# Performance work log

Measured on AMD Instinct MI355X. Metric: run time of the kernel, lower is better.

The kernel has to match this reference:

```python
import jax, jax.numpy as jnp
import numpy as np

S, B, C, H, W = 5, 2, 128, 24, 24
N_ITER = 3
BN_EPS = 1e-5


def conv2d(x, w, b, pad):
    # x: (N, Cin, H, W), w: (Cout, Cin, kh, kw)
    y = jax.lax.conv_general_dilated(
        x, w, (1, 1), [(pad, pad), (pad, pad)],
        dimension_numbers=('NCHW', 'OIHW', 'NCHW'))
    return y + b[None, :, None, None]


def setup_inputs() -> dict:
    key = jax.random.key(0)
    ks = jax.random.split(key, 8)
    sc = 0.03  # keep pre-softmax logits in a sane range
    d = {}
    d['x'] = jax.random.normal(ks[0], (S, B, C, H, W), jnp.float32) * 0.5
    d['Wf_w'] = jax.random.normal(ks[1], (C, C, 3, 3), jnp.float32) * sc
    d['Wf_b'] = jnp.zeros((C,), jnp.float32)
    d['Wh_w'] = jax.random.normal(ks[2], (C, C, 3, 3), jnp.float32) * sc
    d['Wh_b'] = jnp.zeros((C,), jnp.float32)
    d['Wl_w'] = jax.random.normal(ks[3], (C, C, 3, 3), jnp.float32) * sc
    d['Wl_b'] = jnp.zeros((C,), jnp.float32)
    d['alpha'] = jnp.ones((1,), jnp.float32)
    d['Wc'] = jax.random.normal(ks[4], (C, C), jnp.float32) * sc
    d['Wg_w'] = jax.random.normal(ks[5], (C, C, 3, 3), jnp.float32) * sc
    d['Wg_b'] = jnp.zeros((C,), jnp.float32)
    d['bn_gamma'] = jnp.ones((C,), jnp.float32)
    d['bn_beta'] = jnp.zeros((C,), jnp.float32)
    d['gru_zr_w'] = jax.random.normal(ks[6], (2 * C, 2 * C, 5, 5), jnp.float32) * sc
    d['gru_zr_b'] = jnp.zeros((2 * C,), jnp.float32)
    d['gru_h_w'] = jax.random.normal(ks[7], (C, 2 * C, 5, 5), jnp.float32) * sc
    d['gru_h_b'] = jnp.zeros((C,), jnp.float32)
    d['intra_w'] = jnp.full((1,), 0.5, jnp.float32)
    d['inter_w'] = jnp.full((1,), 0.5, jnp.float32)
    return d


def reference(x, Wf_w, Wf_b, Wh_w, Wh_b, Wl_w, Wl_b, alpha, Wc, Wg_w, Wg_b,
              bn_gamma, bn_beta, gru_zr_w, gru_zr_b, gru_h_w, gru_h_b,
              intra_w, inter_w):
    S_, B_, C_, H_, W_ = x.shape
    N = H_ * W_
    # BatchNorm2d in inference mode with fresh running stats (mean=0, var=1)
    bn_scale = bn_gamma / jnp.sqrt(1.0 + BN_EPS)
    mask = (1.0 - jnp.eye(S_, dtype=x.dtype))[:, :, None, None, None, None]
    h = x
    for _ in range(N_ITER):
        hb = h.reshape(S_ * B_, C_, H_, W_)
        # ---- intra-node self-attention (per node in sequence) ----
        ft = conv2d(hb, Wf_w, Wf_b, 1).reshape(S_, B_, C_, N)
        ht = conv2d(hb, Wh_w, Wh_b, 1).reshape(S_, B_, C_, N)
        lt = conv2d(hb, Wl_w, Wl_b, 1).reshape(S_, B_, C_, N)
        att = jax.nn.softmax(jnp.einsum('sbcn,sbcm->sbnm', ft, ht), axis=-1)
        ctx = jnp.einsum('sbnm,sbcm->sbcn', att, lt).reshape(S_, B_, C_, H_, W_)
        eii = alpha[0] * ctx + h
        # ---- inter-node pairwise attention messages (all i,j pairs) ----
        hf = h.reshape(S_, B_, C_, N)
        yt = jnp.einsum('cd,jbdn->jbcn', Wc, hf)
        eij = jnp.einsum('ibcn,jbcm->ijbnm', hf, yt)  # (S,S,B,N,N)
        eijn = jax.nn.softmax(eij, axis=-1)
        mji = jnp.einsum('ijbnm,jbcm->ijbcn', eijn, hf)  # (S,S,B,C,N)
        m4 = mji.reshape(S_ * S_ * B_, C_, H_, W_)
        g = jax.nn.sigmoid(jnp.mean(conv2d(m4, Wg_w, Wg_b, 1),
                                    axis=(2, 3), keepdims=True))
        mg = (g * m4) * bn_scale[None, :, None, None] + bn_beta[None, :, None, None]
        mg = mg.reshape(S_, S_, B_, C_, H_, W_)
        inter = jnp.sum(mg * mask, axis=1)  # exclude j == i
        msg = intra_w[0] * eii + inter_w[0] * inter
        # ---- ConvGRU update + residual ----
        xi = msg.reshape(S_ * B_, C_, H_, W_)
        zr = jax.nn.sigmoid(conv2d(jnp.concatenate([xi, hb], axis=1),
                                   gru_zr_w, gru_zr_b, 2))
        z, r = zr[:, :C_], zr[:, C_:]
        h_hat = jnp.tanh(conv2d(jnp.concatenate([xi, r * hb], axis=1),
                                gru_h_w, gru_h_b, 2))
        h_new = (1.0 - z) * hb + z * h_hat
        h = (h_new + hb).reshape(S_, B_, C_, H_, W_)
    return h
```

## Files before the change

kernel.cpp:

```cpp
#include <hip/hip_runtime.h>
#include <math.h>

#define S_  5
#define B_  2
#define C_  128
#define N_  576
#define SB  10
#define NPAIR 40
#define C2  256

typedef short v8s __attribute__((ext_vector_type(8)));
typedef float v4f __attribute__((ext_vector_type(4)));

#define GLOBAL_AS __attribute__((address_space(1)))
#define LDS_AS    __attribute__((address_space(3)))

__device__ __forceinline__ unsigned short f2bf(float f) {
    union { float f; unsigned u; } v; v.f = f;
    unsigned r = (v.u + 0x7FFF + ((v.u >> 16) & 1)) >> 16;
    return (unsigned short)r;
}
__device__ __forceinline__ float bf2f(unsigned short h) {
    union { unsigned u; float f; } v; v.u = ((unsigned)h) << 16;
    return v.f;
}

__global__ void packA5_kernel(const float* __restrict__ w, unsigned short* __restrict__ Apk, int M)
{
    int idx = blockIdx.x * 256 + threadIdx.x;
    if (idx >= M * 6400) return;
    int r = idx;
    int j = r & 7;      r >>= 3;
    int quad = r & 3;   r >>= 2;
    int l15 = r & 15;   r >>= 4;
    int c = r & 3;      r >>= 2;
    int tap_l = r % 5;  r /= 5;
    int g = r % 5;      r /= 5;
    int ch = r & 1;     r >>= 1;
    int kk = r & 3;     r >>= 2;
    int cgb = r;
    int co = cgb * 64 + c * 16 + l15;
    int ci = kk * 64 + ch * 32 + quad * 8 + j;
    int tap = g * 5 + tap_l;
    Apk[idx] = f2bf(w[((size_t)co * 256 + ci) * 25 + tap]);
}
__global__ void packA3_kernel(const float* __restrict__ wf, const float* __restrict__ wh,
                              const float* __restrict__ wl, unsigned short* __restrict__ Apk)
{
    int idx = blockIdx.x * 256 + threadIdx.x;
    if (idx >= 384 * 1152) return;
    int r = idx;
    int j = r & 7;      r >>= 3;
    int quad = r & 3;   r >>= 2;
    int l15 = r & 15;   r >>= 4;
    int c = r & 3;      r >>= 2;
    int tap_l = r % 3;  r /= 3;
    int g = r % 3;      r /= 3;
    int ch = r & 1;     r >>= 1;
    int kk = r & 1;     r >>= 1;
    int cgb = r;
    int co = cgb * 64 + c * 16 + l15;
    const float* w = (co < 128) ? wf : (co < 256) ? wh : wl;
    int cl = co & 127;
    int ci = kk * 64 + ch * 32 + quad * 8 + j;
    int tap = g * 3 + tap_l;
    Apk[idx] = f2bf(w[((size_t)cl * 128 + ci) * 9 + tap]);
}
__global__ void packWc_kernel(const float* __restrict__ w, unsigned short* __restrict__ o)
{
    int idx = blockIdx.x * 256 + threadIdx.x;
    if (idx < 128 * 128) o[idx] = f2bf(w[idx]);
}
__global__ void packWgT_kernel(const float* __restrict__ w, float* __restrict__ o)
{
    int idx = blockIdx.x * 256 + threadIdx.x;
    if (idx >= 128 * 1152) return;
    int co = idx & 127, i = idx >> 7;
    o[(size_t)i * 128 + co] = w[(size_t)co * 1152 + i];
}

__global__ __launch_bounds__(256) void tc_kernel(
    const float* __restrict__ src, const float* __restrict__ zrp,
    const float* __restrict__ zrb,
    unsigned short* __restrict__ dst, unsigned short* __restrict__ vfd)
{
    const size_t PLANE = (size_t)SB * C2 * N_;
    __shared__ float tile[128][9];
    int img = blockIdx.y, px0 = blockIdx.x * 8, t = threadIdx.x;
    #pragma unroll
    for (int i = 0; i < 4; ++i) {
        int e = i * 256 + t; int ci = e >> 3; int px = e & 7;
        float v = src[((size_t)img * 128 + ci) * 576 + px0 + px];
        if (zrp) {
            size_t zi = ((size_t)img * C2 + 128 + ci) * 576 + px0 + px;
            float a = zrb[128 + ci];
            #pragma unroll
            for (int k = 0; k < 4; ++k) a += zrp[k * PLANE + zi];
            v *= 1.f / (1.f + __expf(-a));
        }
        tile[ci][px] = v;
        if (vfd) {
            int m = px0 + px;
            int ctile = ci >> 4, l15v = ci & 15;
            int sIdx = m >> 5, quadv = (m >> 3) & 3, j = m & 7;
            vfd[(((size_t)img * 8 + ctile) * 18 + sIdx) * 512 + (quadv * 16 + l15v) * 8 + j] = f2bf(v);
        }
    }
    __syncthreads();
    #pragma unroll
    for (int i = 0; i < 4; ++i) {
        int e = i * 256 + t; int pxl = e >> 7; int ci = e & 127;
        dst[((size_t)img * 576 + px0 + pxl) * 128 + ci] = f2bf(tile[ci][pxl]);
    }
}

template<int KD, int R, int CINT, int SPLITK, int MODE>
__global__ __launch_bounds__(256, 1) void conv_mfma(
    const unsigned short* __restrict__ srcA, const unsigned short* __restrict__ srcB,
    const unsigned short* __restrict__ Apk, int COUT, float* __restrict__ po,
    const float* __restrict__ b0, const float* __restrict__ b1, const float* __restrict__ b2,
    unsigned short* __restrict__ t0, unsigned short* __restrict__ t1,
    unsigned short* __restrict__ t2)
{
    constexpr int PART   = CINT / SPLITK;
    constexpr int NCH    = PART / 32;
    constexpr int NSUB   = NCH * KD;
    constexpr int WR     = 8 + 2 * R;
    constexpr int WC     = 24 + 2 * R;
    constexpr int NPOS   = WR * WC;
    constexpr int NSLOTB = NPOS * 4;
    constexpr int RB     = (NSLOTB + 255) / 256;
    constexpr int AUNITS = KD * 4 * 64;
    constexpr int AR     = AUNITS / 256;
    __shared__ __align__(16) unsigned short Ab[2][AUNITS * 8];
    __shared__ __align__(16) unsigned short Bb[NPOS * 32];

    int f   = blockIdx.x;
    int kk  = f % SPLITK;
    int cgb = f / SPLITK;
    int pxb = blockIdx.y;
    int img = blockIdx.z;
    int t = threadIdx.x;
    int wave = t >> 6, lane = t & 63;
    int quad = lane >> 4, l15 = lane & 15;
    int r0 = pxb * 8;

    const int cibase = kk * PART;
    const unsigned short* src = (cibase >= 128) ? srcB : srcA;
    const int cioff0 = cibase & 127;
    const unsigned short* srcI = src + (size_t)img * 576 * 128;

    int posBase[3], pxs[3];
    #pragma unroll
    for (int s = 0; s < 3; ++s) {
        int px = pxb * 192 + wave * 48 + s * 16 + l15;
        pxs[s] = px;
        int pr = px / 24, pc = px % 24;
        posBase[s] = (pr - r0 + R) * WC + pc + R;
    }

    int goffB[RB]; bool gokB[RB];
    #pragma unroll
    for (int rr = 0; rr < RB; ++rr) {
        int idx = rr * 256 + wave * 64 + lane;
        int pos = idx >> 2, slotq = idx & 3;
        int gr = slotq ^ ((pos >> 1) & 3);
        int wr = pos / WC, wc = pos % WC;
        int grow = r0 - R + wr, gcol = wc - R;
        gokB[rr] = (idx < NSLOTB) && grow >= 0 && grow < 24 && gcol >= 0 && gcol < 24;
        goffB[rr] = (grow * 24 + gcol) * 128 + gr * 8;
    }

    auto stageB = [&](int ch) {
        const unsigned short* sp = srcI + cioff0 + ch * 32;
        #pragma unroll
        for (int rr = 0; rr < RB; ++rr) {
            if (gokB[rr]) {
                __builtin_amdgcn_global_load_lds(
                    (const GLOBAL_AS void*)(sp + goffB[rr]),
                    (LDS_AS void*)((char*)&Bb[0] + (size_t)(rr * 256 + wave * 64) * 16),
                    16, 0, 0);
            }
        }
    };
    auto stageA = [&](int sub, int buf) {
        const unsigned short* sp = Apk + ((size_t)((cgb * SPLITK + kk) * NSUB + sub)) * (AUNITS * 8);
        #pragma unroll
        for (int r = 0; r < AR; ++r) {
            int u0 = r * 256 + wave * 64;
            __builtin_amdgcn_global_load_lds(
                (const GLOBAL_AS void*)(sp + (size_t)(u0 + lane) * 8),
                (LDS_AS void*)((char*)&Ab[buf][0] + (size_t)u0 * 16),
                16, 0, 0);
        }
    };

    v4f acc[4][3];
    #pragma unroll
    for (int c = 0; c < 4; ++c)
        #pragma unroll
        for (int s = 0; s < 3; ++s)
            #pragma unroll
            for (int r = 0; r < 4; ++r) acc[c][s][r] = 0.f;

    {
        v8s zv;
        #pragma unroll
        for (int j = 0; j < 8; ++j) zv[j] = 0;
        for (int i = t; i < NPOS * 4; i += 256) ((v8s*)Bb)[i] = zv;
    }
    __syncthreads();
    stageB(0);
    stageA(0, 0);
    __syncthreads();

    int sub = 0;
    #pragma unroll 1
    for (int ch = 0; ch < NCH; ++ch) {
        #pragma unroll 1
        for (int g = 0; g < KD; ++g) {
            if (sub + 1 < NSUB) stageA(sub + 1, (sub + 1) & 1);
            const unsigned short* Ap = &Ab[sub & 1][0];
            #pragma unroll
            for (int tl = 0; tl < KD; ++tl) {
                int doff = (g - R) * WC + (tl - R);
                v8s a[4];
                #pragma unroll
                for (int c = 0; c < 4; ++c)
                    a[c] = *(const v8s*)&Ap[((tl * 4 + c) * 64 + l15 * 4 + quad) * 8];
                v8s b[3];
                #pragma unroll
                for (int s = 0; s < 3; ++s) {
                    int pos = posBase[s] + doff;
                    b[s] = *(const v8s*)&Bb[pos * 32 + ((quad ^ ((pos >> 1) & 3)) << 3)];
                }
                #pragma unroll
                for (int c = 0; c < 4; ++c)
                    #pragma unroll
                    for (int s = 0; s < 3; ++s)
                        acc[c][s] = __builtin_amdgcn_mfma_f32_16x16x32_bf16(a[c], b[s], acc[c][s], 0, 0, 0);
            }
            __syncthreads();
            ++sub;
        }
        if (ch + 1 < NCH) { stageB(ch + 1); __syncthreads(); }
    }

    if (MODE == 0) {
        float* out = po + (size_t)kk * ((size_t)SB * COUT * 576)
                   + ((size_t)img * COUT + cgb * 64) * 576;
        #pragma unroll
        for (int c = 0; c < 4; ++c)
            #pragma unroll
            for (int s = 0; s < 3; ++s)
                #pragma unroll
                for (int r = 0; r < 4; ++r) {
                    int col = c * 16 + quad * 4 + r;
                    out[(size_t)col * 576 + pxs[s]] = acc[c][s][r];
                }
    } else {
        #pragma unroll
        for (int c = 0; c < 4; ++c)
            #pragma unroll
            for (int s = 0; s < 3; ++s) {
                int px = pxs[s];
                #pragma unroll
                for (int r = 0; r < 4; ++r) {
                    int co = cgb * 64 + c * 16 + quad * 4 + r;
                    int which = co >> 7, cl = co & 127;
                    const float* bp = (which == 0) ? b0 : (which == 1) ? b1 : b2;
                    float v = acc[c][s][r] + bp[cl];
                    if (which == 0) {
                        t0[((size_t)img * 576 + px) * 128 + cl] = f2bf(v);
                    } else if (which == 1) {
                        int mt = px >> 4, l15m = px & 15;
                        int kb = cl >> 5, quadk = (cl >> 3) & 3, jj = cl & 7;
                        t1[(((size_t)img * 36 + mt) * 4 + kb) * 512 + (quadk * 16 + l15m) * 8 + jj] = f2bf(v);
                    } else {
                        int ctile = cl >> 4, l15v = cl & 15;
                        int sIdx = px >> 5, quadv = (px >> 3) & 3, jj = px & 7;
                        t2[(((size_t)img * 8 + ctile) * 18 + sIdx) * 512 + (quadv * 16 + l15v) * 8 + jj] = f2bf(v);
                    }
                }
            }
    }
}

__global__ __launch_bounds__(256) void yt_mfma(
    const unsigned short* __restrict__ hT, const unsigned short* __restrict__ Wcb,
    unsigned short* __restrict__ KFi)
{
    int t = threadIdx.x, wave = t >> 6, lane = t & 63;
    int q = lane >> 4, l15 = lane & 15;
    int n0 = blockIdx.x * 16, img = blockIdx.y;
    v4f acc[2];
    #pragma unroll
    for (int ct = 0; ct < 2; ++ct)
        #pragma unroll
        for (int r = 0; r < 4; ++r) acc[ct][r] = 0.f;
    #pragma unroll
    for (int kk = 0; kk < 4; ++kk) {
        v8s b = *(const v8s*)(hT + ((size_t)img * 576 + n0 + l15) * 128 + kk * 32 + q * 8);
        #pragma unroll
        for (int ct = 0; ct < 2; ++ct) {
            v8s a = *(const v8s*)(Wcb + (size_t)((wave * 2 + ct) * 16 + l15) * 128 + kk * 32 + q * 8);
            acc[ct] = __builtin_amdgcn_mfma_f32_16x16x32_bf16(a, b, acc[ct], 0, 0, 0);
        }
    }
    int mt = blockIdx.x;
    #pragma unroll
    for (int ct = 0; ct < 2; ++ct) {
        #pragma unroll
        for (int r = 0; r < 4; ++r) {
            int co = (wave * 2 + ct) * 16 + q * 4 + r;
            int kk = co >> 5, quadk = (co >> 3) & 3, j = co & 7;
            KFi[(((size_t)img * 36 + mt) * 4 + kk) * 512 + (quadk * 16 + l15) * 8 + j]
                = f2bf(acc[ct][r]);
        }
    }
}

template<int MODE>
__global__ __launch_bounds__(256) void attn_mfma(
    const unsigned short* __restrict__ QT, const unsigned short* __restrict__ KF,
    const unsigned short* __restrict__ VF, float* __restrict__ Of,
    unsigned short* __restrict__ Oh, const float* __restrict__ addsrc,
    const float* __restrict__ alpha)
{
    __shared__ __align__(16) unsigned short P[16 * 576];
    __shared__ float redmx[4][16];
    __shared__ float redsm[4][16];
    int t = threadIdx.x;
    int wave = t >> 6, lane = t & 63;
    int q = lane >> 4, l15 = lane & 15;
    int n0 = blockIdx.x * 16;
    int p = blockIdx.y;
    int qimg, kimg;
    if (MODE == 0) { qimg = p; kimg = p; }
    else {
        int b = p & 1; int ij = p >> 1; int i = ij >> 2; int jj = ij & 3;
        int j = jj + (jj >= i ? 1 : 0);
        qimg = i * 2 + b; kimg = j * 2 + b;
    }
    const unsigned short* Qp = QT + ((size_t)qimg * 576 + n0) * 128;
    const unsigned short* Kp = KF + (size_t)kimg * 36 * 4 * 512;
    const unsigned short* Vp = VF + (size_t)kimg * 8 * 18 * 512;

    v8s aq[4];
    #pragma unroll
    for (int kk = 0; kk < 4; ++kk)
        aq[kk] = *(const v8s*)(Qp + (size_t)l15 * 128 + kk * 32 + q * 8);

    v4f S[9];
    #pragma unroll
    for (int i = 0; i < 9; ++i)
        #pragma unroll
        for (int r = 0; r < 4; ++r) S[i][r] = 0.f;

    #pragma unroll
    for (int i = 0; i < 9; ++i) {
        int mt = wave * 9 + i;
        #pragma unroll
        for (int kk = 0; kk < 4; ++kk) {
            v8s b = *(const v8s*)(Kp + ((size_t)(mt * 4 + kk)) * 512 + lane * 8);
            S[i] = __builtin_amdgcn_mfma_f32_16x16x32_bf16(aq[kk], b, S[i], 0, 0, 0);
        }
    }

    float mx[4];
    #pragma unroll
    for (int r = 0; r < 4; ++r) {
        float m = S[0][r];
        #pragma unroll
        for (int i = 1; i < 9; ++i) m = fmaxf(m, S[i][r]);
        #pragma unroll
        for (int off = 1; off < 16; off <<= 1) m = fmaxf(m, __shfl_xor(m, off));
        mx[r] = m;
    }
    if (l15 == 0) {
        #pragma unroll
        for (int r = 0; r < 4; ++r) redmx[wave][q * 4 + r] = mx[r];
    }
    __syncthreads();
    float sum[4];
    #pragma unroll
    for (int r = 0; r < 4; ++r) {
        float g = fmaxf(fmaxf(redmx[0][q * 4 + r], redmx[1][q * 4 + r]),
                        fmaxf(redmx[2][q * 4 + r], redmx[3][q * 4 + r]));
        float s = 0.f;
        #pragma unroll
        for (int i = 0; i < 9; ++i) { float e = __expf(S[i][r] - g); S[i][r] = e; s += e; }
        #pragma unroll
        for (int off = 1; off < 16; off <<= 1) s += __shfl_xor(s, off);
        sum[r] = s;
    }
    if (l15 == 0) {
        #pragma unroll
        for (int r = 0; r < 4; ++r) redsm[wave][q * 4 + r] = sum[r];
    }
    #pragma unroll
    for (int i = 0; i < 9; ++i) {
        int m = (wave * 9 + i) * 16 + l15;
        int cm = m >> 3, mo = m & 7;
        #pragma unroll
        for (int r = 0; r < 4; ++r) {
            int n = q * 4 + r;
            P[n * 576 + ((cm ^ (n & 7)) << 3) + mo] = f2bf(S[i][r]);
        }
    }
    __syncthreads();
    float inv[4];
    #pragma unroll
    for (int r = 0; r < 4; ++r)
        inv[r] = 1.f / (redsm[0][q * 4 + r] + redsm[1][q * 4 + r] +
                        redsm[2][q * 4 + r] + redsm[3][q * 4 + r]);

    v4f o[2];
    #pragma unroll
    for (int ct = 0; ct < 2; ++ct)
        #pragma unroll
        for (int r = 0; r < 4; ++r) o[ct][r] = 0.f;

    for (int s = 0; s < 18; ++s) {
        int cm = s * 4 + q;
        v8s a = *(const v8s*)&P[l15 * 576 + ((cm ^ (l15 & 7)) << 3)];
        #pragma unroll
        for (int ct = 0; ct < 2; ++ct) {
            int ctile = wave * 2 + ct;
            v8s b = *(const v8s*)(Vp + ((size_t)(ctile * 18 + s)) * 512 + lane * 8);
            o[ct] = __builtin_amdgcn_mfma_f32_16x16x32_bf16(a, b, o[ct], 0, 0, 0);
        }
    }

    #pragma unroll
    for (int ct = 0; ct < 2; ++ct) {
        int c = (wave * 2 + ct) * 16 + l15;
        size_t base = ((size_t)p * 128 + c) * 576 + n0 + q * 4;
        if (MODE == 0) {
            float al = alpha[0];
            #pragma unroll
            for (int r = 0; r < 4; ++r)
                Of[base + r] = al * o[ct][r] * inv[r] + addsrc[base + r];
        } else {
            #pragma unroll
            for (int r = 0; r < 4; ++r)
                Oh[base + r] = f2bf(o[ct][r] * inv[r]);
        }
    }
}

__global__ __launch_bounds__(64) void wsum_kernel(
    const unsigned short* __restrict__ mji, float* __restrict__ wsum)
{
    int pair = blockIdx.x, ci = blockIdx.y, lane = threadIdx.x;
    const unsigned short* p = mji + ((size_t)pair * C_ + ci) * N_;
    float T=0, R0=0, R23=0, Cl=0, Cr=0, c00=0, c0w=0, ch0=0, chw=0;
    for (int i = lane; i < N_; i += 64) {
        float v = bf2f(p[i]);
        int r = i / 24, cc = i % 24;
        T += v;
        if (r == 0)  R0  += v;
        if (r == 23) R23 += v;
        if (cc == 0)  Cl += v;
        if (cc == 23) Cr += v;
        if (i == 0)   c00 = v;
        if (i == 23)  c0w = v;
        if (i == 552) ch0 = v;
        if (i == 575) chw = v;
    }
    #pragma unroll
    for (int off = 32; off > 0; off >>= 1) {
        T  += __shfl_xor(T, off);  R0 += __shfl_xor(R0, off);  R23 += __shfl_xor(R23, off);
        Cl += __shfl_xor(Cl, off); Cr += __shfl_xor(Cr, off);
        c00 += __shfl_xor(c00, off); c0w += __shfl_xor(c0w, off);
        ch0 += __shfl_xor(ch0, off); chw += __shfl_xor(chw, off);
    }
    if (lane == 0) {
        float rowsub[3] = {R23, 0.f, R0};
        float colsub[3] = {Cr,  0.f, Cl};
        float corner[9] = {chw, 0.f, ch0,  0.f, 0.f, 0.f,  c0w, 0.f, c00};
        float* o = wsum + ((size_t)pair * C_ + ci) * 9;
        #pragma unroll
        for (int ky = 0; ky < 3; ++ky)
            #pragma unroll
            for (int kx = 0; kx < 3; ++kx)
                o[ky * 3 + kx] = T - rowsub[ky] - colsub[kx] + corner[ky * 3 + kx];
    }
}

__global__ __launch_bounds__(128) void g_kernel(
    const float* __restrict__ wsum, const float* __restrict__ WgT,
    const float* __restrict__ Wgb, float* __restrict__ g)
{
    __shared__ float sw[C_ * 9];
    int pair = blockIdx.x; int co = threadIdx.x;
    for (int i = co; i < C_ * 9; i += 128) sw[i] = wsum[(size_t)pair * C_ * 9 + i];
    __syncthreads();
    float acc = 0.f;
    for (int i = 0; i < C_ * 9; ++i) acc += WgT[(size_t)i * 128 + co] * sw[i];
    float m = acc * (1.f / 576.f) + Wgb[co];
    g[pair * C_ + co] = 1.f / (1.f + __expf(-m));
}

__global__ __launch_bounds__(256) void msg_tc_kernel(
    const float* __restrict__ eii, const unsigned short* __restrict__ mji,
    const float* __restrict__ g, const float* __restrict__ bn_gamma,
    const float* __restrict__ bn_beta, const float* __restrict__ intra_w,
    const float* __restrict__ inter_w, unsigned short* __restrict__ msgT)
{
    __shared__ float tile[128][9];
    int img = blockIdx.y, px0 = blockIdx.x * 8, t = threadIdx.x;
    int s = img >> 1, b = img & 1;
    float iw = intra_w[0], ew = inter_w[0];
    #pragma unroll
    for (int i = 0; i < 4; ++i) {
        int e = i * 256 + t; int ci = e >> 3; int pxl = e & 7;
        int px = px0 + pxl;
        float scale = bn_gamma[ci] * rsqrtf(1.f + 1e-5f);
        float acc = 0.f;
        #pragma unroll
        for (int jj = 0; jj < 4; ++jj) {
            int pidx = (s * 4 + jj) * 2 + b;
            acc += g[pidx * C_ + ci] * bf2f(mji[((size_t)pidx * C_ + ci) * N_ + px]);
        }
        float inter = scale * acc + 4.f * bn_beta[ci];
        tile[ci][pxl] = iw * eii[((size_t)img * C_ + ci) * N_ + px] + ew * inter;
    }
    __syncthreads();
    #pragma unroll
    for (int i = 0; i < 4; ++i) {
        int e = i * 256 + t; int pxl = e >> 7; int ci = e & 127;
        msgT[((size_t)img * 576 + px0 + pxl) * 128 + ci] = f2bf(tile[ci][pxl]);
    }
}

__global__ __launch_bounds__(256) void update_tc_kernel(
    const float* __restrict__ zrp, const float* __restrict__ zrb,
    const float* __restrict__ hhp, const float* __restrict__ ghb,
    const float* __restrict__ h, float* __restrict__ out,
    unsigned short* __restrict__ hTn, unsigned short* __restrict__ VFn, int last)
{
    const size_t ZP = (size_t)SB * C2 * N_;
    const size_t HP = (size_t)SB * C_ * N_;
    __shared__ float tile[128][9];
    int img = blockIdx.y, px0 = blockIdx.x * 8, t = threadIdx.x;
    #pragma unroll
    for (int i = 0; i < 4; ++i) {
        int e = i * 256 + t; int ci = e >> 3; int pxl = e & 7;
        int px = px0 + pxl;
        size_t zi = ((size_t)img * C2 + ci) * N_ + px;
        float za = zrb[ci];
        #pragma unroll
        for (int k = 0; k < 4; ++k) za += zrp[k * ZP + zi];
        float z = 1.f / (1.f + __expf(-za));
        size_t hi = ((size_t)img * C_ + ci) * N_ + px;
        float ha = ghb[ci];
        #pragma unroll
        for (int k = 0; k < 4; ++k) ha += hhp[k * HP + hi];
        float hh = tanhf(ha);
        float o = (2.f - z) * h[hi] + z * hh;
        out[hi] = o;
        tile[ci][pxl] = o;
        if (!last) {
            int ctile = ci >> 4, l15v = ci & 15;
            int sIdx = px >> 5, quadv = (px >> 3) & 3, j = px & 7;
            VFn[(((size_t)img * 8 + ctile) * 18 + sIdx) * 512 + (quadv * 16 + l15v) * 8 + j] = f2bf(o);
        }
    }
    if (!last) {
        __syncthreads();
        #pragma unroll
        for (int i = 0; i < 4; ++i) {
            int e = i * 256 + t; int pxl = e >> 7; int ci = e & 127;
            hTn[((size_t)img * 576 + px0 + pxl) * 128 + ci] = f2bf(tile[ci][pxl]);
        }
    }
}

extern "C" void kernel_launch(void* const* d_in, const int* in_sizes, int n_in,
                              void* d_out, int out_size, void* d_ws, size_t ws_size,
                              hipStream_t stream)
{
    const float* x      = (const float*)d_in[0];
    const float* Wf_w   = (const float*)d_in[1];
    const float* Wf_b   = (const float*)d_in[2];
    const float* Wh_w   = (const float*)d_in[3];
    const float* Wh_b   = (const float*)d_in[4];
    const float* Wl_w   = (const float*)d_in[5];
    const float* Wl_b   = (const float*)d_in[6];
    const float* alpha  = (const float*)d_in[7];
    const float* Wc     = (const float*)d_in[8];
    const float* Wg_w   = (const float*)d_in[9];
    const float* Wg_b   = (const float*)d_in[10];
    const float* bng    = (const float*)d_in[11];
    const float* bnb    = (const float*)d_in[12];
    const float* zr_w   = (const float*)d_in[13];
    const float* zr_b   = (const float*)d_in[14];
    const float* gh_w   = (const float*)d_in[15];
    const float* gh_b   = (const float*)d_in[16];
    const float* intraw = (const float*)d_in[17];
    const float* interw = (const float*)d_in[18];
    float* outp = (float*)d_out;

    float* f = (float*)d_ws;
    const size_t SZ = (size_t)SB * C_ * N_;
    float* hbuf  = f; f += SZ;
    float* eii   = f; f += SZ;
    float* zrp   = f; f += 4 * (size_t)SB * C2 * N_;
    float* hhp   = f; f += 4 * SZ;
    float* wsumb = f; f += (size_t)NPAIR * C_ * 9;
    float* gbuf  = f; f += (size_t)NPAIR * C_;
    float* WgT   = f; f += (size_t)128 * 1152;
    unsigned short* us = (unsigned short*)f;
    unsigned short* mji16  = us; us += (size_t)NPAIR * C_ * N_;
    unsigned short* hT16   = us; us += SZ;
    unsigned short* hc16   = us; us += SZ;
    unsigned short* msgT16 = us; us += SZ;
    unsigned short* ftT    = us; us += SZ;
    unsigned short* KFa    = us; us += SZ;
    unsigned short* VFa    = us; us += SZ;
    unsigned short* Wp3    = us; us += (size_t)384 * 1152;
    unsigned short* Wpzr   = us; us += (size_t)256 * 6400;
    unsigned short* Wph    = us; us += (size_t)128 * 6400;
    unsigned short* Wcb    = us; us += (size_t)128 * 128;

    unsigned short* KFi    = ftT;
    unsigned short* VFi    = hc16;
    unsigned short* rhbT16 = hc16;

    packA3_kernel<<<(384 * 1152 + 255) / 256, 256, 0, stream>>>(Wf_w, Wh_w, Wl_w, Wp3);
    packA5_kernel<<<(256 * 6400 + 255) / 256, 256, 0, stream>>>(zr_w, Wpzr, 256);
    packA5_kernel<<<(128 * 6400 + 255) / 256, 256, 0, stream>>>(gh_w, Wph, 128);
    packWc_kernel<<<64, 256, 0, stream>>>(Wc, Wcb);
    packWgT_kernel<<<(128 * 1152 + 255) / 256, 256, 0, stream>>>(Wg_w, WgT);

    tc_kernel<<<dim3(72, SB), 256, 0, stream>>>(x, nullptr, nullptr, hT16, VFi);

    const float* hcur = x;
    for (int it = 0; it < 3; ++it) {
        float* hout = (it == 2) ? outp : hbuf;

        conv_mfma<3, 1, 128, 1, 1><<<dim3(6, 3, SB), 256, 0, stream>>>(
            hT16, hT16, Wp3, 384, nullptr, Wf_b, Wh_b, Wl_b, ftT, KFa, VFa);
        attn_mfma<0><<<dim3(36, SB), 256, 0, stream>>>(ftT, KFa, VFa, eii, nullptr, hcur, alpha);
        yt_mfma<<<dim3(36, SB), 256, 0, stream>>>(hT16, Wcb, KFi);
        attn_mfma<1><<<dim3(36, NPAIR), 256, 0, stream>>>(hT16, KFi, VFi, nullptr, mji16, nullptr, nullptr);
        wsum_kernel<<<dim3(NPAIR, C_), 64, 0, stream>>>(mji16, wsumb);
        g_kernel<<<NPAIR, 128, 0, stream>>>(wsumb, WgT, Wg_b, gbuf);
        msg_tc_kernel<<<dim3(72, SB), 256, 0, stream>>>(eii, mji16, gbuf, bng, bnb, intraw, interw, msgT16);
        conv_mfma<5, 2, 256, 4, 0><<<dim3(16, 3, SB), 256, 0, stream>>>(
            msgT16, hT16, Wpzr, 256, zrp, nullptr, nullptr, nullptr, nullptr, nullptr, nullptr);
        tc_kernel<<<dim3(72, SB), 256, 0, stream>>>(hcur, zrp, zr_b, rhbT16, nullptr);
        conv_mfma<5, 2, 256, 4, 0><<<dim3(8, 3, SB), 256, 0, stream>>>(
            msgT16, rhbT16, Wph, 128, hhp, nullptr, nullptr, nullptr, nullptr, nullptr, nullptr);
        update_tc_kernel<<<dim3(72, SB), 256, 0, stream>>>(
            zrp, zr_b, hhp, gh_b, hcur, hout, hT16, VFi, (it == 2) ? 1 : 0);
        hcur = hout;
    }
}
```

Before: 619.1 us.

## Merge pack, conv3+yt, intra/inter attention launches and fold wsum into attention

Folds the five weight-pack kernels and the initial transpose into one launch, runs the 3x3 conv alongside the yt projection in a single grid, and merges the intra and inter attention into one grid. The wsum reduction kernel is removed: the inter-attention epilogue now writes per-tile partial border sums, and g_kernel reduces these. The aim is fewer launches and less idle time between dependent small kernels. In exchange KFi needs its own buffer, g_kernel reads a larger partial-sum array, and the merged grids mix blocks with different cost.

```diff
diff --git a/kernel.cpp b/kernel.cpp
--- a/kernel.cpp
+++ b/kernel.cpp
@@ -25,9 +25,9 @@
     return v.f;
 }
 
-__global__ void packA5_kernel(const float* __restrict__ w, unsigned short* __restrict__ Apk, int M)
-{
-    int idx = blockIdx.x * 256 + threadIdx.x;
+__device__ __forceinline__ void packA5_body(int idx, const float* __restrict__ w,
+                                            unsigned short* __restrict__ Apk, int M)
+{
     if (idx >= M * 6400) return;
     int r = idx;
     int j = r & 7;      r >>= 3;
@@ -44,10 +44,11 @@
     int tap = g * 5 + tap_l;
     Apk[idx] = f2bf(w[((size_t)co * 256 + ci) * 25 + tap]);
 }
-__global__ void packA3_kernel(const float* __restrict__ wf, const float* __restrict__ wh,
-                              const float* __restrict__ wl, unsigned short* __restrict__ Apk)
-{
-    int idx = blockIdx.x * 256 + threadIdx.x;
+__device__ __forceinline__ void packA3_body(int idx, const float* __restrict__ wf,
+                                            const float* __restrict__ wh,
+                                            const float* __restrict__ wl,
+                                            unsigned short* __restrict__ Apk)
+{
     if (idx >= 384 * 1152) return;
     int r = idx;
     int j = r & 7;      r >>= 3;
@@ -66,27 +67,28 @@
     int tap = g * 3 + tap_l;
     Apk[idx] = f2bf(w[((size_t)cl * 128 + ci) * 9 + tap]);
 }
-__global__ void packWc_kernel(const float* __restrict__ w, unsigned short* __restrict__ o)
-{
-    int idx = blockIdx.x * 256 + threadIdx.x;
+__device__ __forceinline__ void packWc_body(int idx, const float* __restrict__ w,
+                                            unsigned short* __restrict__ o)
+{
     if (idx < 128 * 128) o[idx] = f2bf(w[idx]);
 }
-__global__ void packWgT_kernel(const float* __restrict__ w, float* __restrict__ o)
-{
-    int idx = blockIdx.x * 256 + threadIdx.x;
+__device__ __forceinline__ void packWgT_body(int idx, const float* __restrict__ w,
+                                             float* __restrict__ o)
+{
     if (idx >= 128 * 1152) return;
     int co = idx & 127, i = idx >> 7;
     o[(size_t)i * 128 + co] = w[(size_t)co * 1152 + i];
 }
 
-__global__ __launch_bounds__(256) void tc_kernel(
+__device__ __forceinline__ void tc_body(
+    int px0, int img,
     const float* __restrict__ src, const float* __restrict__ zrp,
     const float* __restrict__ zrb,
     unsigned short* __restrict__ dst, unsigned short* __restrict__ vfd)
 {
     const size_t PLANE = (size_t)SB * C2 * N_;
     __shared__ float tile[128][9];
-    int img = blockIdx.y, px0 = blockIdx.x * 8, t = threadIdx.x;
+    int t = threadIdx.x;
     #pragma unroll
     for (int i = 0; i < 4; ++i) {
         int e = i * 256 + t; int ci = e >> 3; int px = e & 7;
@@ -114,8 +116,50 @@
     }
 }
 
+__global__ __launch_bounds__(256) void tc_kernel(
+    const float* __restrict__ src, const float* __restrict__ zrp,
+    const float* __restrict__ zrb,
+    unsigned short* __restrict__ dst, unsigned short* __restrict__ vfd)
+{
+    tc_body(blockIdx.x * 8, blockIdx.y, src, zrp, zrb, dst, vfd);
+}
+
+#define NB_A3   1728
+#define NB_A5ZR 6400
+#define NB_A5H  3200
+#define NB_WC   64
+#define NB_WGT  576
+#define NB_TC   720
+__global__ __launch_bounds__(256) void pack_all_kernel(
+    const float* __restrict__ Wf_w, const float* __restrict__ Wh_w,
+    const float* __restrict__ Wl_w, unsigned short* __restrict__ Wp3,
+    const float* __restrict__ zr_w, unsigned short* __restrict__ Wpzr,
+    const float* __restrict__ gh_w, unsigned short* __restrict__ Wph,
+    const float* __restrict__ Wc,  unsigned short* __restrict__ Wcb,
+    const float* __restrict__ Wg_w, float* __restrict__ WgT,
+    const float* __restrict__ x, unsigned short* __restrict__ hT16,
+    unsigned short* __restrict__ VFi)
+{
+    int bid = blockIdx.x, t = threadIdx.x;
+    if (bid < NB_A3) {
+        packA3_body(bid * 256 + t, Wf_w, Wh_w, Wl_w, Wp3);
+    } else if (bid < NB_A3 + NB_A5ZR) {
+        packA5_body((bid - NB_A3) * 256 + t, zr_w, Wpzr, 256);
+    } else if (bid < NB_A3 + NB_A5ZR + NB_A5H) {
+        packA5_body((bid - NB_A3 - NB_A5ZR) * 256 + t, gh_w, Wph, 128);
+    } else if (bid < NB_A3 + NB_A5ZR + NB_A5H + NB_WC) {
+        packWc_body((bid - NB_A3 - NB_A5ZR - NB_A5H) * 256 + t, Wc, Wcb);
+    } else if (bid < NB_A3 + NB_A5ZR + NB_A5H + NB_WC + NB_WGT) {
+        packWgT_body((bid - NB_A3 - NB_A5ZR - NB_A5H - NB_WC) * 256 + t, Wg_w, WgT);
+    } else {
+        int b2 = bid - (NB_A3 + NB_A5ZR + NB_A5H + NB_WC + NB_WGT);
+        tc_body((b2 % 72) * 8, b2 / 72, x, nullptr, nullptr, hT16, VFi);
+    }
+}
+
 template<int KD, int R, int CINT, int SPLITK, int MODE>
-__global__ __launch_bounds__(256, 1) void conv_mfma(
+__device__ __forceinline__ void conv_body(
+    int bx, int by, int bz,
     const unsigned short* __restrict__ srcA, const unsigned short* __restrict__ srcB,
     const unsigned short* __restrict__ Apk, int COUT, float* __restrict__ po,
     const float* __restrict__ b0, const float* __restrict__ b1, const float* __restrict__ b2,
@@ -135,11 +179,11 @@
     __shared__ __align__(16) unsigned short Ab[2][AUNITS * 8];
     __shared__ __align__(16) unsigned short Bb[NPOS * 32];
 
-    int f   = blockIdx.x;
+    int f   = bx;
     int kk  = f % SPLITK;
     int cgb = f / SPLITK;
-    int pxb = blockIdx.y;
-    int img = blockIdx.z;
+    int pxb = by;
+    int img = bz;
     int t = threadIdx.x;
     int wave = t >> 6, lane = t & 63;
     int quad = lane >> 4, l15 = lane & 15;
@@ -286,13 +330,26 @@
     }
 }
 
-__global__ __launch_bounds__(256) void yt_mfma(
+template<int KD, int R, int CINT, int SPLITK, int MODE>
+__global__ __launch_bounds__(256, 1) void conv_mfma(
+    const unsigned short* __restrict__ srcA, const unsigned short* __restrict__ srcB,
+    const unsigned short* __restrict__ Apk, int COUT, float* __restrict__ po,
+    const float* __restrict__ b0, const float* __restrict__ b1, const float* __restrict__ b2,
+    unsigned short* __restrict__ t0, unsigned short* __restrict__ t1,
+    unsigned short* __restrict__ t2)
+{
+    conv_body<KD, R, CINT, SPLITK, MODE>(blockIdx.x, blockIdx.y, blockIdx.z,
+        srcA, srcB, Apk, COUT, po, b0, b1, b2, t0, t1, t2);
+}
+
+__device__ __forceinline__ void yt_body(
+    int mt, int img,
     const unsigned short* __restrict__ hT, const unsigned short* __restrict__ Wcb,
     unsigned short* __restrict__ KFi)
 {
     int t = threadIdx.x, wave = t >> 6, lane = t & 63;
     int q = lane >> 4, l15 = lane & 15;
-    int n0 = blockIdx.x * 16, img = blockIdx.y;
+    int n0 = mt * 16;
     v4f acc[2];
     #pragma unroll
     for (int ct = 0; ct < 2; ++ct)
@@ -307,7 +364,6 @@
             acc[ct] = __builtin_amdgcn_mfma_f32_16x16x32_bf16(a, b, acc[ct], 0, 0, 0);
         }
     }
-    int mt = blockIdx.x;
     #pragma unroll
     for (int ct = 0; ct < 2; ++ct) {
         #pragma unroll
@@ -320,12 +376,31 @@
     }
 }
 
-template<int MODE>
-__global__ __launch_bounds__(256) void attn_mfma(
-    const unsigned short* __restrict__ QT, const unsigned short* __restrict__ KF,
-    const unsigned short* __restrict__ VF, float* __restrict__ Of,
-    unsigned short* __restrict__ Oh, const float* __restrict__ addsrc,
-    const float* __restrict__ alpha)
+__global__ __launch_bounds__(256, 1) void conv3_yt_kernel(
+    const unsigned short* __restrict__ hT, const unsigned short* __restrict__ Wp3,
+    const float* __restrict__ Wf_b, const float* __restrict__ Wh_b,
+    const float* __restrict__ Wl_b,
+    unsigned short* __restrict__ ftT, unsigned short* __restrict__ KFa,
+    unsigned short* __restrict__ VFa,
+    const unsigned short* __restrict__ Wcb, unsigned short* __restrict__ KFi)
+{
+    int bid = blockIdx.x;
+    if (bid < 180) {
+        conv_body<3, 1, 128, 1, 1>(bid % 6, (bid / 6) % 3, bid / 18,
+            hT, hT, Wp3, 384, nullptr, Wf_b, Wh_b, Wl_b, ftT, KFa, VFa);
+    } else {
+        int b2 = bid - 180;
+        yt_body(b2 % 36, b2 / 36, hT, Wcb, KFi);
+    }
+}
+
+__global__ __launch_bounds__(256) void attn_merged(
+    const unsigned short* __restrict__ QTi, const unsigned short* __restrict__ KFa,
+    const unsigned short* __restrict__ VFa, float* __restrict__ Of,
+    const float* __restrict__ addsrc, const float* __restrict__ alpha,
+    const unsigned short* __restrict__ QTe, const unsigned short* __restrict__ KFe,
+    const unsigned short* __restrict__ VFe, unsigned short* __restrict__ Oh,
+    float* __restrict__ wpart)
 {
     __shared__ __align__(16) unsigned short P[16 * 576];
     __shared__ float redmx[4][16];
@@ -333,18 +408,25 @@
     int t = threadIdx.x;
     int wave = t >> 6, lane = t & 63;
     int q = lane >> 4, l15 = lane & 15;
-    int n0 = blockIdx.x * 16;
+    int mt = blockIdx.x;
+    int n0 = mt * 16;
     int p = blockIdx.y;
-    int qimg, kimg;
-    if (MODE == 0) { qimg = p; kimg = p; }
-    else {
-        int b = p & 1; int ij = p >> 1; int i = ij >> 2; int jj = ij & 3;
+    bool intra = (p < SB);
+    int pp = 0;
+    const unsigned short *Qp, *Kp, *Vp;
+    if (intra) {
+        Qp = QTi + ((size_t)p * 576 + n0) * 128;
+        Kp = KFa + (size_t)p * 36 * 4 * 512;
+        Vp = VFa + (size_t)p * 8 * 18 * 512;
+    } else {
+        pp = p - SB;
+        int b = pp & 1; int ij = pp >> 1; int i = ij >> 2; int jj = ij & 3;
         int j = jj + (jj >= i ? 1 : 0);
-        qimg = i * 2 + b; kimg = j * 2 + b;
-    }
-    const unsigned short* Qp = QT + ((size_t)qimg * 576 + n0) * 128;
-    const unsigned short* Kp = KF + (size_t)kimg * 36 * 4 * 512;
-    const unsigned short* Vp = VF + (size_t)kimg * 8 * 18 * 512;
+        int qimg = i * 2 + b, kimg = j * 2 + b;
+        Qp = QTe + ((size_t)qimg * 576 + n0) * 128;
+        Kp = KFe + (size_t)kimg * 36 * 4 * 512;
+        Vp = VFe + (size_t)kimg * 8 * 18 * 512;
+    }
 
     v8s aq[4];
     #pragma unroll
@@ -359,10 +441,10 @@
 
     #pragma unroll
     for (int i = 0; i < 9; ++i) {
-        int mt = wave * 9 + i;
+        int mtk = wave * 9 + i;
         #pragma unroll
         for (int kk = 0; kk < 4; ++kk) {
-            v8s b = *(const v8s*)(Kp + ((size_t)(mt * 4 + kk)) * 512 + lane * 8);
+            v8s b = *(const v8s*)(Kp + ((size_t)(mtk * 4 + kk)) * 512 + lane * 8);
             S[i] = __builtin_amdgcn_mfma_f32_16x16x32_bf16(aq[kk], b, S[i], 0, 0, 0);
         }
     }
@@ -432,69 +514,82 @@
         }
     }
 
-    #pragma unroll
-    for (int ct = 0; ct < 2; ++ct) {
-        int c = (wave * 2 + ct) * 16 + l15;
-        size_t base = ((size_t)p * 128 + c) * 576 + n0 + q * 4;
-        if (MODE == 0) {
-            float al = alpha[0];
+    if (intra) {
+        float al = alpha[0];
+        #pragma unroll
+        for (int ct = 0; ct < 2; ++ct) {
+            int c = (wave * 2 + ct) * 16 + l15;
+            size_t base = ((size_t)p * 128 + c) * 576 + n0 + q * 4;
             #pragma unroll
             for (int r = 0; r < 4; ++r)
                 Of[base + r] = al * o[ct][r] * inv[r] + addsrc[base + r];
-        } else {
-            #pragma unroll
-            for (int r = 0; r < 4; ++r)
-                Oh[base + r] = f2bf(o[ct][r] * inv[r]);
-        }
-    }
-}
-
-__global__ __launch_bounds__(64) void wsum_kernel(
-    const unsigned short* __restrict__ mji, float* __restrict__ wsum)
-{
-    int pair = blockIdx.x, ci = blockIdx.y, lane = threadIdx.x;
-    const unsigned short* p = mji + ((size_t)pair * C_ + ci) * N_;
-    float T=0, R0=0, R23=0, Cl=0, Cr=0, c00=0, c0w=0, ch0=0, chw=0;
-    for (int i = lane; i < N_; i += 64) {
-        float v = bf2f(p[i]);
-        int r = i / 24, cc = i % 24;
-        T += v;
-        if (r == 0)  R0  += v;
-        if (r == 23) R23 += v;
-        if (cc == 0)  Cl += v;
-        if (cc == 23) Cr += v;
-        if (i == 0)   c00 = v;
-        if (i == 23)  c0w = v;
-        if (i == 552) ch0 = v;
-        if (i == 575) chw = v;
-    }
-    #pragma unroll
-    for (int off = 32; off > 0; off >>= 1) {
-        T  += __shfl_xor(T, off);  R0 += __shfl_xor(R0, off);  R23 += __shfl_xor(R23, off);
-        Cl += __shfl_xor(Cl, off); Cr += __shfl_xor(Cr, off);
-        c00 += __shfl_xor(c00, off); c0w += __shfl_xor(c0w, off);
-        ch0 += __shfl_xor(ch0, off); chw += __shfl_xor(chw, off);
-    }
-    if (lane == 0) {
-        float rowsub[3] = {R23, 0.f, R0};
-        float colsub[3] = {Cr,  0.f, Cl};
-        float corner[9] = {chw, 0.f, ch0,  0.f, 0.f, 0.f,  c0w, 0.f, c00};
-        float* o = wsum + ((size_t)pair * C_ + ci) * 9;
-        #pragma unroll
-        for (int ky = 0; ky < 3; ++ky)
-            #pragma unroll
-            for (int kx = 0; kx < 3; ++kx)
-                o[ky * 3 + kx] = T - rowsub[ky] - colsub[kx] + corner[ky * 3 + kx];
+        }
+    } else {
+        #pragma unroll
+        for (int ct = 0; ct < 2; ++ct) {
+            int c = (wave * 2 + ct) * 16 + l15;
+            size_t base = ((size_t)pp * 128 + c) * 576 + n0 + q * 4;
+            float vr[4];
+            #pragma unroll
+            for (int r = 0; r < 4; ++r) {
+                unsigned short hb = f2bf(o[ct][r] * inv[r]);
+                Oh[base + r] = hb;
+                vr[r] = bf2f(hb);
+            }
+            float sums[9];
+            #pragma unroll
+            for (int k = 0; k < 9; ++k) sums[k] = 0.f;
+            #pragma unroll
+            for (int r = 0; r < 4; ++r) {
+                int px = n0 + q * 4 + r;
+                int row = px / 24, col = px % 24;
+                float v = vr[r];
+                sums[0] += v;
+                if (row == 0)  sums[1] += v;
+                if (row == 23) sums[2] += v;
+                if (col == 0)  sums[3] += v;
+                if (col == 23) sums[4] += v;
+                if (px == 0)   sums[5] += v;
+                if (px == 23)  sums[6] += v;
+                if (px == 552) sums[7] += v;
+                if (px == 575) sums[8] += v;
+            }
+            #pragma unroll
+            for (int k = 0; k < 9; ++k) {
+                sums[k] += __shfl_xor(sums[k], 16);
+                sums[k] += __shfl_xor(sums[k], 32);
+            }
+            if (q == 0) {
+                float* wp = wpart + (((size_t)pp * 36 + mt) * 9) * 128 + c;
+                #pragma unroll
+                for (int k = 0; k < 9; ++k) wp[k * 128] = sums[k];
+            }
+        }
     }
 }
 
 __global__ __launch_bounds__(128) void g_kernel(
-    const float* __restrict__ wsum, const float* __restrict__ WgT,
+    const float* __restrict__ wpart, const float* __restrict__ WgT,
     const float* __restrict__ Wgb, float* __restrict__ g)
 {
     __shared__ float sw[C_ * 9];
     int pair = blockIdx.x; int co = threadIdx.x;
-    for (int i = co; i < C_ * 9; i += 128) sw[i] = wsum[(size_t)pair * C_ * 9 + i];
+    float raw[9];
+    #pragma unroll
+    for (int k = 0; k < 9; ++k) raw[k] = 0.f;
+    const float* base = wpart + (size_t)pair * 36 * 9 * 128 + co;
+    for (int mt = 0; mt < 36; ++mt) {
+        #pragma unroll
+        for (int k = 0; k < 9; ++k) raw[k] += base[(mt * 9 + k) * 128];
+    }
+    float rowsub[3] = {raw[2], 0.f, raw[1]};
+    float colsub[3] = {raw[4], 0.f, raw[3]};
+    float corner[9] = {raw[8], 0.f, raw[7], 0.f, 0.f, 0.f, raw[6], 0.f, raw[5]};
+    #pragma unroll
+    for (int ky = 0; ky < 3; ++ky)
+        #pragma unroll
+        for (int kx = 0; kx < 3; ++kx)
+            sw[co * 9 + ky * 3 + kx] = raw[0] - rowsub[ky] - colsub[kx] + corner[ky * 3 + kx];
     __syncthreads();
     float acc = 0.f;
     for (int i = 0; i < C_ * 9; ++i) acc += WgT[(size_t)i * 128 + co] * sw[i];
@@ -608,7 +703,7 @@
     float* eii   = f; f += SZ;
     float* zrp   = f; f += 4 * (size_t)SB * C2 * N_;
     float* hhp   = f; f += 4 * SZ;
-    float* wsumb = f; f += (size_t)NPAIR * C_ * 9;
+    float* wpart = f; f += (size_t)NPAIR * 36 * 9 * 128;
     float* gbuf  = f; f += (size_t)NPAIR * C_;
     float* WgT   = f; f += (size_t)128 * 1152;
     unsigned short* us = (unsigned short*)f;
@@ -623,31 +718,26 @@
     unsigned short* Wpzr   = us; us += (size_t)256 * 6400;
     unsigned short* Wph    = us; us += (size_t)128 * 6400;
     unsigned short* Wcb    = us; us += (size_t)128 * 128;
-
-    unsigned short* KFi    = ftT;
+    unsigned short* KFi    = us; us += SZ;
+
     unsigned short* VFi    = hc16;
     unsigned short* rhbT16 = hc16;
 
-    packA3_kernel<<<(384 * 1152 + 255) / 256, 256, 0, stream>>>(Wf_w, Wh_w, Wl_w, Wp3);
-    packA5_kernel<<<(256 * 6400 + 255) / 256, 256, 0, stream>>>(zr_w, Wpzr, 256);
-    packA5_kernel<<<(128 * 6400 + 255) / 256, 256, 0, stream>>>(gh_w, Wph, 128);
-    packWc_kernel<<<64, 256, 0, stream>>>(Wc, Wcb);
-    packWgT_kernel<<<(128 * 1152 + 255) / 256, 256, 0, stream>>>(Wg_w, WgT);
-
-    tc_kernel<<<dim3(72, SB), 256, 0, stream>>>(x, nullptr, nullptr, hT16, VFi);
+    pack_all_kernel<<<NB_A3 + NB_A5ZR + NB_A5H + NB_WC + NB_WGT + NB_TC, 256, 0, stream>>>(
+        Wf_w, Wh_w, Wl_w, Wp3, zr_w, Wpzr, gh_w, Wph, Wc, Wcb, Wg_w, WgT,
+        x, hT16, VFi);
 
     const float* hcur = x;
     for (int it = 0; it < 3; ++it) {
         float* hout = (it == 2) ? outp : hbuf;
 
-        conv_mfma<3, 1, 128, 1, 1><<<dim3(6, 3, SB), 256, 0, stream>>>(
-            hT16, hT16, Wp3, 384, nullptr, Wf_b, Wh_b, Wl_b, ftT, KFa, VFa);
-        attn_mfma<0><<<dim3(36, SB), 256, 0, stream>>>(ftT, KFa, VFa, eii, nullptr, hcur, alpha);
-        yt_mfma<<<dim3(36, SB), 256, 0, stream>>>(hT16, Wcb, KFi);
-        attn_mfma<1><<<dim3(36, NPAIR), 256, 0, stream>>>(hT16, KFi, VFi, nullptr, mji16, nullptr, nullptr);
-        wsum_kernel<<<dim3(NPAIR, C_), 64, 0, stream>>>(mji16, wsumb);
-        g_kernel<<<NPAIR, 128, 0, stream>>>(wsumb, WgT, Wg_b, gbuf);
-        msg_tc_kernel<<<dim3(72, SB), 256, 0, stream>>>(eii, mji16, gbuf, bng, bnb, intraw, interw, msgT16);
+        conv3_yt_kernel<<<540, 256, 0, stream>>>(
+            hT16, Wp3, Wf_b, Wh_b, Wl_b, ftT, KFa, VFa, Wcb, KFi);
+        attn_merged<<<dim3(36, SB + NPAIR), 256, 0, stream>>>(
+            ftT, KFa, VFa, eii, hcur, alpha, hT16, KFi, VFi, mji16, wpart);
+        g_kernel<<<NPAIR, 128, 0, stream>>>(wpart, WgT, Wg_b, gbuf);
+        msg_tc_kernel<<<dim3(72, SB), 256, 0, stream>>>(
+            eii, mji16, gbuf, bng, bnb, intraw, interw, msgT16);
         conv_mfma<5, 2, 256, 4, 0><<<dim3(16, 3, SB), 256, 0, stream>>>(
             msgT16, hT16, Wpzr, 256, zrp, nullptr, nullptr, nullptr, nullptr, nullptr, nullptr);
         tc_kernel<<<dim3(72, SB), 256, 0, stream>>>(hcur, zrp, zr_b, rhbT16, nullptr);
```

New measurement: 568.4 us. 1.09x faster.
